# Optimization experiments

Measured on AMD Instinct MI355X. Metric: run time of the kernel, lower is better.

The kernel has to match this reference:

```python
import jax, jax.numpy as jnp
import numpy as np

EPS = 1e-8
INTRA_MARGIN_USED = 1.5  # combine() swaps margins: intra gets delta_dist
INTER_MARGIN_USED = 0.5  # inter gets delta_var
INTRA_W, INTER_W, REG_W = 1.0, 1.0, 0.001


def setup_inputs() -> dict:
    key = jax.random.key(0)
    k1, k2 = jax.random.split(key)
    N, D, K = 1000000, 32, 64
    features = jax.random.normal(k1, (N, D), dtype=jnp.float32)
    labels = jax.random.randint(k2, (N,), 0, K, dtype=jnp.int64 if jax.config.jax_enable_x64 else jnp.int32)
    return {"features": features, "labels": labels, "num_clusters": K}


def reference(features, labels, num_clusters):
    K = int(num_clusters)
    N, D = features.shape
    ones = jnp.ones((N,), dtype=features.dtype)
    counts = jax.ops.segment_sum(ones, labels, num_segments=K)            # (K,)
    sums = jax.ops.segment_sum(features, labels, num_segments=K)          # (K, D)
    safe_counts = jnp.maximum(counts, 1.0)
    means = sums / safe_counts[:, None]                                   # (K, D) cluster centroids

    # --- intra (variance) loss; margin = 1.5 due to original swap ---
    diff = features - means[labels] + EPS                                 # (N, D)
    dists = jnp.sqrt(jnp.sum(diff * diff, axis=1))                        # (N,)
    hinge2 = jnp.square(jnp.maximum(dists - INTRA_MARGIN_USED, 0.0))
    per_cluster = jax.ops.segment_sum(hinge2, labels, num_segments=K) / safe_counts
    intra_loss = jnp.mean(per_cluster)

    # --- inter (distance) loss; margin = 0.5 due to original swap ---
    pdiff = means[:, None, :] - means[None, :, :] + EPS                   # (K, K, D)
    pdist = jnp.sqrt(jnp.sum(pdiff * pdiff, axis=-1))                     # (K, K)
    hinge = jnp.square(jnp.maximum(2.0 * INTER_MARGIN_USED - pdist, 0.0))
    offdiag = 1.0 - jnp.eye(K, dtype=features.dtype)
    inter_loss = jnp.sum(hinge * offdiag) / float((K - 1) * K)

    # --- regularization ---
    reg_loss = jnp.mean(jnp.sqrt(jnp.sum(jnp.square(means + EPS), axis=1)))

    total = INTRA_W * intra_loss + INTER_W * inter_loss + REG_W * reg_loss
    return total
```

## Files before the change

kernel.cpp:

```cpp
#include <hip/hip_runtime.h>
#include <math.h>


#define EPS_F 1e-8f
constexpr int D = 32;
constexpr int K = 64;
constexpr int NPTS = 1024;
constexpr int P1 = K * D + K;
constexpr int NCH = 64;
constexpr int NBLK2 = 2048;
constexpr int MPAD = 40;

__global__ __launch_bounds__(256, 4) void pass1_kernel(
    const float* __restrict__ feat, const int* __restrict__ lab,
    float* __restrict__ part1, int N)
{
    __shared__ int            s_lab[NPTS];
    __shared__ unsigned short s_idx[NPTS];
    __shared__ int            s_hist[K];
    __shared__ int            s_pref[K];
    __shared__ int            s_cur[K];

    const int tid = threadIdx.x;
    const long long base = (long long)blockIdx.x * NPTS;
    int npts = (int)((long long)N - base);
    if (npts > NPTS) npts = NPTS;

    if (tid < K) s_hist[tid] = 0;
    __syncthreads();

    const int n4 = npts >> 2;
    for (int i4 = tid; i4 < n4; i4 += 256) {
        const int4 v = ((const int4*)(lab + base))[i4];
        s_lab[i4 * 4 + 0] = v.x; s_lab[i4 * 4 + 1] = v.y;
        s_lab[i4 * 4 + 2] = v.z; s_lab[i4 * 4 + 3] = v.w;
        atomicAdd(&s_hist[v.x], 1); atomicAdd(&s_hist[v.y], 1);
        atomicAdd(&s_hist[v.z], 1); atomicAdd(&s_hist[v.w], 1);
    }
    for (int i = (n4 << 2) + tid; i < npts; i += 256) {
        const int l = lab[base + i];
        s_lab[i] = l;
        atomicAdd(&s_hist[l], 1);
    }
    __syncthreads();

    if (tid < 64) {
        const int h = s_hist[tid];
        int v = h;
        for (int off = 1; off < 64; off <<= 1) {
            const int up = __shfl_up(v, off);
            if (tid >= off) v += up;
        }
        s_pref[tid] = v - h;
        s_cur[tid]  = v - h;
    }
    __syncthreads();

    for (int i = tid; i < npts; i += 256) {
        const int l = s_lab[i];
        const int pos = atomicAdd(&s_cur[l], 1);
        s_idx[pos] = (unsigned short)i;
    }
    __syncthreads();

    const int k = tid >> 2, q = tid & 3;
    const int start = s_pref[k], len = s_hist[k];
    float4 a0 = {0.f, 0.f, 0.f, 0.f}, a1 = {0.f, 0.f, 0.f, 0.f};
    int i = 0;
    for (; i + 4 <= len; i += 4) {
        const int i0 = s_idx[start + i + 0];
        const int i1 = s_idx[start + i + 1];
        const int i2 = s_idx[start + i + 2];
        const int i3 = s_idx[start + i + 3];
        const float4* r0 = (const float4*)(feat + (base + i0) * D + q * 8);
        const float4* r1 = (const float4*)(feat + (base + i1) * D + q * 8);
        const float4* r2 = (const float4*)(feat + (base + i2) * D + q * 8);
        const float4* r3 = (const float4*)(feat + (base + i3) * D + q * 8);
        const float4 x0 = r0[0], y0 = r0[1];
        const float4 x1 = r1[0], y1 = r1[1];
        const float4 x2 = r2[0], y2 = r2[1];
        const float4 x3 = r3[0], y3 = r3[1];
        a0.x += (x0.x + x1.x) + (x2.x + x3.x);
        a0.y += (x0.y + x1.y) + (x2.y + x3.y);
        a0.z += (x0.z + x1.z) + (x2.z + x3.z);
        a0.w += (x0.w + x1.w) + (x2.w + x3.w);
        a1.x += (y0.x + y1.x) + (y2.x + y3.x);
        a1.y += (y0.y + y1.y) + (y2.y + y3.y);
        a1.z += (y0.z + y1.z) + (y2.z + y3.z);
        a1.w += (y0.w + y1.w) + (y2.w + y3.w);
    }
    for (; i < len; ++i) {
        const int i0 = s_idx[start + i];
        const float4* r0 = (const float4*)(feat + (base + i0) * D + q * 8);
        const float4 x0 = r0[0], y0 = r0[1];
        a0.x += x0.x; a0.y += x0.y; a0.z += x0.z; a0.w += x0.w;
        a1.x += y0.x; a1.y += y0.y; a1.z += y0.z; a1.w += y0.w;
    }
    float* outp = part1 + (long long)blockIdx.x * P1;
    ((float4*)outp)[tid * 2 + 0] = a0;
    ((float4*)outp)[tid * 2 + 1] = a1;
    if (tid < K) outp[K * D + tid] = (float)s_hist[tid];
}

__global__ __launch_bounds__(256) void reduce1_kernel(
    const float* __restrict__ part1, float* __restrict__ part2,
    int chsz, int nblk1)
{
    const int e = blockIdx.x * 256 + threadIdx.x;
    if (e >= P1) return;
    const int y = blockIdx.y;
    const int b0 = y * chsz;
    int b1 = b0 + chsz; if (b1 > nblk1) b1 = nblk1;
    float s = 0.f;
    for (int b = b0; b < b1; b++) s += part1[(long long)b * P1 + e];
    part2[(long long)y * P1 + e] = s;
}

__global__ __launch_bounds__(256) void mean_kernel(
    const float* __restrict__ part2,
    float* __restrict__ means, float* __restrict__ icnt)
{
    const int e = blockIdx.x * blockDim.x + threadIdx.x;
    if (e >= P1) return;
    if (e < K * D) {
        float s = 0.f, c = 0.f;
        const int k = e >> 5;
        for (int y = 0; y < NCH; y++) {
            s += part2[(long long)y * P1 + e];
            c += part2[(long long)y * P1 + K * D + k];
        }
        means[e] = s / fmaxf(c, 1.0f);
    } else {
        float s = 0.f;
        for (int y = 0; y < NCH; y++) s += part2[(long long)y * P1 + e];
        icnt[e - K * D] = 1.0f / fmaxf(s, 1.0f);
    }
}

__global__ __launch_bounds__(256, 4) void pass2_kernel(
    const float* __restrict__ feat, const int* __restrict__ lab,
    const float* __restrict__ means, const float* __restrict__ icnt,
    float* __restrict__ hpart, float* __restrict__ ir, int N)
{
    __shared__ float s_m[K * MPAD];
    __shared__ float s_ic[K];
    __shared__ float s_red[256];
    const int tid = threadIdx.x;

    for (int e = tid; e < K * D; e += 256)
        s_m[(e >> 5) * MPAD + (e & 31)] = means[e];
    if (tid < K) s_ic[tid] = icnt[tid];
    __syncthreads();

    float racc = 0.f;
    const long long stride = (long long)NBLK2 * 256;
    for (long long p = (long long)blockIdx.x * 256 + tid; p < N; p += stride) {
        const int l = lab[p];
        const float4* frow = (const float4*)(feat + p * D);
        float4 fv[8];
        #pragma unroll
        for (int j = 0; j < 8; j++) fv[j] = frow[j];
        const float* mrow = s_m + l * MPAD;
        float d2 = 0.f;
        #pragma unroll
        for (int j = 0; j < 8; j++) {
            const float4 mv = *(const float4*)(mrow + j * 4);
            const float dx = fv[j].x - mv.x + EPS_F;
            const float dy = fv[j].y - mv.y + EPS_F;
            const float dz = fv[j].z - mv.z + EPS_F;
            const float dw = fv[j].w - mv.w + EPS_F;
            d2 += dx * dx + dy * dy + dz * dz + dw * dw;
        }
        const float h = fmaxf(sqrtf(d2) - 1.5f, 0.f);
        racc += h * h * s_ic[l];
    }
    s_red[tid] = racc;
    __syncthreads();
    for (int st = 128; st; st >>= 1) { if (tid < st) s_red[tid] += s_red[tid + st]; __syncthreads(); }
    if (tid == 0) hpart[blockIdx.x] = s_red[0];

    if (blockIdx.x != 0) return;
    __syncthreads();
    float mj[32];
    const int j = tid & 63;
    #pragma unroll
    for (int d = 0; d < 32; d++) mj[d] = s_m[j * MPAD + d];
    float isum = 0.f;
    const int igrp = tid >> 6;
    for (int ii = 0; ii < 16; ii++) {
        const int i = igrp * 16 + ii;
        const float4* srow = (const float4*)(s_m + i * MPAD);
        float d2 = 0.f;
        #pragma unroll
        for (int q = 0; q < 8; q++) {
            const float4 mv = srow[q];
            const float b0 = mv.x - mj[q * 4 + 0] + EPS_F;
            const float b1 = mv.y - mj[q * 4 + 1] + EPS_F;
            const float b2 = mv.z - mj[q * 4 + 2] + EPS_F;
            const float b3 = mv.w - mj[q * 4 + 3] + EPS_F;
            d2 += b0 * b0 + b1 * b1 + b2 * b2 + b3 * b3;
        }
        if (i != j) {
            const float h = fmaxf(1.0f - sqrtf(d2), 0.f);
            isum += h * h;
        }
    }
    s_red[tid] = isum;
    __syncthreads();
    for (int st = 128; st; st >>= 1) { if (tid < st) s_red[tid] += s_red[tid + st]; __syncthreads(); }
    if (tid == 0) ir[0] = s_red[0] * (1.0f / ((K - 1) * K));
    __syncthreads();

    float r = 0.f;
    if (tid < 64) {
        float d2 = 0.f;
        #pragma unroll
        for (int d = 0; d < 32; d++) { const float t = mj[d] + EPS_F; d2 += t * t; }
        r = sqrtf(d2);
    }
    s_red[tid] = r;
    __syncthreads();
    for (int st = 128; st; st >>= 1) { if (tid < st) s_red[tid] += s_red[tid + st]; __syncthreads(); }
    if (tid == 0) ir[1] = s_red[0] * (1.0f / K);
}

__global__ __launch_bounds__(256) void final_kernel(
    const float* __restrict__ hpart, const float* __restrict__ ir,
    float* __restrict__ out)
{
    __shared__ float s_red[256];
    const int tid = threadIdx.x;
    float hs = 0.f;
    for (int b = tid; b < NBLK2; b += 256) hs += hpart[b];
    s_red[tid] = hs;
    __syncthreads();
    for (int st = 128; st; st >>= 1) { if (tid < st) s_red[tid] += s_red[tid + st]; __syncthreads(); }
    if (tid == 0) out[0] = s_red[0] * (1.0f / K) + ir[0] + 0.001f * ir[1];
}

extern "C" void kernel_launch(void* const* d_in, const int* in_sizes, int n_in,
                              void* d_out, int out_size, void* d_ws, size_t ws_size,
                              hipStream_t stream)
{
    const float* feat = (const float*)d_in[0];
    const int*   lab  = (const int*)d_in[1];
    const int N = in_sizes[1];

    float* ws = (float*)d_ws;

    const int nblk1 = (N + NPTS - 1) / NPTS;
    const int chsz  = (nblk1 + NCH - 1) / NCH;

    float* means = ws;
    float* icnt  = means + K * D;
    float* ir    = icnt + K;
    float* part2 = ir + 4;
    float* hpart = part2 + (long long)NCH * P1;
    float* part1 = hpart + NBLK2;

    pass1_kernel<<<nblk1, 256, 0, stream>>>(feat, lab, part1, N);
    reduce1_kernel<<<dim3((P1 + 255) / 256, NCH), 256, 0, stream>>>(part1, part2, chsz, nblk1);
    mean_kernel<<<(P1 + 255) / 256, 256, 0, stream>>>(part2, means, icnt);
    pass2_kernel<<<NBLK2, 256, 0, stream>>>(feat, lab, means, icnt, hpart, ir, N);
    final_kernel<<<1, 256, 0, stream>>>(hpart, ir, (float*)d_out);
}
```

Before: 65.76 us.

## Merge partial reduction kernels into one means kernel and double points per block

Replaces the two-stage reduce1/mean reduction of per-block partials with a single means_kernel that has one block per cluster plus one block for counts, each reducing over all pass1 partials in shared memory. NPTS doubles, so pass1 emits half as many partials. This removes one kernel launch and the intermediate part2 buffer. It risks fewer pass1 blocks hiding memory latency less well, and leaves the reduction on only 65 blocks.

```diff
diff --git a/kernel.cpp b/kernel.cpp
--- a/kernel.cpp
+++ b/kernel.cpp
@@ -5,9 +5,8 @@
 #define EPS_F 1e-8f
 constexpr int D = 32;
 constexpr int K = 64;
-constexpr int NPTS = 1024;
+constexpr int NPTS = 2048;
 constexpr int P1 = K * D + K;
-constexpr int NCH = 64;
 constexpr int NBLK2 = 2048;
 constexpr int MPAD = 40;
 
@@ -102,38 +101,41 @@
     if (tid < K) outp[K * D + tid] = (float)s_hist[tid];
 }
 
-__global__ __launch_bounds__(256) void reduce1_kernel(
-    const float* __restrict__ part1, float* __restrict__ part2,
-    int chsz, int nblk1)
-{
-    const int e = blockIdx.x * 256 + threadIdx.x;
-    if (e >= P1) return;
-    const int y = blockIdx.y;
-    const int b0 = y * chsz;
-    int b1 = b0 + chsz; if (b1 > nblk1) b1 = nblk1;
-    float s = 0.f;
-    for (int b = b0; b < b1; b++) s += part1[(long long)b * P1 + e];
-    part2[(long long)y * P1 + e] = s;
-}
-
-__global__ __launch_bounds__(256) void mean_kernel(
-    const float* __restrict__ part2,
+__global__ __launch_bounds__(256) void means_kernel(
+    const float* __restrict__ part1, int nblk1,
     float* __restrict__ means, float* __restrict__ icnt)
 {
-    const int e = blockIdx.x * blockDim.x + threadIdx.x;
-    if (e >= P1) return;
-    if (e < K * D) {
+    __shared__ float s_s[256];
+    __shared__ float s_c[256];
+    const int tid = threadIdx.x;
+    const int bid = blockIdx.x;
+    if (bid < K) {
+        const int el = tid & 31, y = tid >> 5;
         float s = 0.f, c = 0.f;
-        const int k = e >> 5;
-        for (int y = 0; y < NCH; y++) {
-            s += part2[(long long)y * P1 + e];
-            c += part2[(long long)y * P1 + K * D + k];
-        }
-        means[e] = s / fmaxf(c, 1.0f);
+        for (int b = y; b < nblk1; b += 8) {
+            const float* pb = part1 + (long long)b * P1;
+            s += pb[bid * 32 + el];
+            c += pb[K * D + bid];
+        }
+        s_s[tid] = s; s_c[tid] = c;
+        __syncthreads();
+        for (int off = 128; off >= 32; off >>= 1) {
+            if (tid < off) { s_s[tid] += s_s[tid + off]; s_c[tid] += s_c[tid + off]; }
+            __syncthreads();
+        }
+        if (tid < 32) means[bid * 32 + tid] = s_s[tid] / fmaxf(s_c[tid], 1.0f);
     } else {
-        float s = 0.f;
-        for (int y = 0; y < NCH; y++) s += part2[(long long)y * P1 + e];
-        icnt[e - K * D] = 1.0f / fmaxf(s, 1.0f);
+        const int el = tid & 63, y = tid >> 6;
+        float c = 0.f;
+        for (int b = y; b < nblk1; b += 4)
+            c += part1[(long long)b * P1 + K * D + el];
+        s_c[tid] = c;
+        __syncthreads();
+        for (int off = 128; off >= 64; off >>= 1) {
+            if (tid < off) s_c[tid] += s_c[tid + off];
+            __syncthreads();
+        }
+        if (tid < 64) icnt[el] = 1.0f / fmaxf(s_c[tid], 1.0f);
     }
 }
 
@@ -249,18 +251,15 @@
     float* ws = (float*)d_ws;
 
     const int nblk1 = (N + NPTS - 1) / NPTS;
-    const int chsz  = (nblk1 + NCH - 1) / NCH;
 
     float* means = ws;
     float* icnt  = means + K * D;
     float* ir    = icnt + K;
-    float* part2 = ir + 4;
-    float* hpart = part2 + (long long)NCH * P1;
+    float* hpart = ir + 4;
     float* part1 = hpart + NBLK2;
 
     pass1_kernel<<<nblk1, 256, 0, stream>>>(feat, lab, part1, N);
-    reduce1_kernel<<<dim3((P1 + 255) / 256, NCH), 256, 0, stream>>>(part1, part2, chsz, nblk1);
-    mean_kernel<<<(P1 + 255) / 256, 256, 0, stream>>>(part2, means, icnt);
+    means_kernel<<<K + 1, 256, 0, stream>>>(part1, nblk1, means, icnt);
     pass2_kernel<<<NBLK2, 256, 0, stream>>>(feat, lab, means, icnt, hpart, ir, N);
     final_kernel<<<1, 256, 0, stream>>>(hpart, ir, (float*)d_out);
 }
```

Measured after the change: 73.36 us. +11.6%, slower.
